# Kernel tuning notes

Measured on AMD Instinct MI355X. Metric: run time of the kernel, lower is better.

Reference implementation:

```python
import jax, jax.numpy as jnp
import numpy as np

N = 50000
E = 1600000
IN_CH = 128
HID = 16
HEADS = 8
OUT_CH = 1
NEG_SLOPE = 0.2


def setup_inputs() -> dict:
    key = jax.random.key(0)
    ks = jax.random.split(key, 12)
    x = jax.random.normal(ks[0], (N, IN_CH), dtype=jnp.float32)
    edge_index = jax.random.randint(ks[1], (2, E), 0, N, dtype=jnp.int64)
    s1 = 1.0 / np.sqrt(IN_CH)
    s2 = 1.0 / np.sqrt(HEADS * HID)
    W1 = jax.random.normal(ks[2], (IN_CH, HEADS * HID), dtype=jnp.float32) * s1
    att_src1 = jax.random.normal(ks[3], (HEADS, HID), dtype=jnp.float32) * s1
    att_dst1 = jax.random.normal(ks[4], (HEADS, HID), dtype=jnp.float32) * s1
    b1 = jnp.zeros((HEADS * HID,), dtype=jnp.float32)
    W2 = jax.random.normal(ks[5], (HEADS * HID, OUT_CH), dtype=jnp.float32) * s2
    att_src2 = jax.random.normal(ks[6], (1, OUT_CH), dtype=jnp.float32) * s2
    att_dst2 = jax.random.normal(ks[7], (1, OUT_CH), dtype=jnp.float32) * s2
    b2 = jnp.zeros((OUT_CH,), dtype=jnp.float32)
    return {"x": x, "edge_index": edge_index,
            "W1": W1, "att_src1": att_src1, "att_dst1": att_dst1, "b1": b1,
            "W2": W2, "att_src2": att_src2, "att_dst2": att_dst2, "b2": b2}


def gat_conv(x, src, dst, W, att_src, att_dst, b, heads, concat):
    n = x.shape[0]
    h = (x @ W).reshape(n, heads, -1)               # [N, H, C]
    a_s = jnp.einsum('nhc,hc->nh', h, att_src)      # [N, H]
    a_d = jnp.einsum('nhc,hc->nh', h, att_dst)
    e = jax.nn.leaky_relu(a_s[src] + a_d[dst], NEG_SLOPE)  # [E, H]
    # segment softmax over incoming edges of each dst node
    emax = jax.ops.segment_max(e, dst, num_segments=n)
    p = jnp.exp(e - emax[dst])
    denom = jax.ops.segment_sum(p, dst, num_segments=n)
    alpha = p / (denom[dst] + 1e-16)                 # [E, H]
    msg = h[src] * alpha[:, :, None]                 # [E, H, C]
    out = jax.ops.segment_sum(msg, dst, num_segments=n)  # [N, H, C]
    if concat:
        out = out.reshape(n, -1)
    else:
        out = out.mean(axis=1)
    return out + b


def reference(x, edge_index, W1, att_src1, att_dst1, b1, W2, att_src2, att_dst2, b2):
    n = x.shape[0]
    loops = jnp.arange(n, dtype=edge_index.dtype)
    src = jnp.concatenate([edge_index[0], loops])    # PyG add_self_loops=True
    dst = jnp.concatenate([edge_index[1], loops])
    h = gat_conv(x, src, dst, W1, att_src1, att_dst1, b1, HEADS, True)
    h = jax.nn.elu(h)
    out = gat_conv(h, src, dst, W2, att_src2, att_dst2, b2, 1, False)
    return out
```

## Files before the change

kernel.cpp:

```cpp
#include <hip/hip_runtime.h>
#include <hip/hip_fp16.h>
#include <math.h>

#define N_NODES 50000
#define N_EDGES 1600000
#define NEG 0.2f

#define PB 256
#define CHUNK (N_EDGES / PB)
#define EPT 25
#define BSHIFT 4
#define NBUCK (N_NODES >> BSHIFT)
#define STRIDE 768
#define GEMMB ((N_NODES + 31) / 32)


__global__ __launch_bounds__(256) void scatter_gemm(const int* __restrict__ ei, int* __restrict__ bcnt,
                                                    int* __restrict__ temp,
                                                    const float* __restrict__ x, const float* __restrict__ W1,
                                                    const float* __restrict__ att_s, const float* __restrict__ att_d,
                                                    __half2* __restrict__ h1, float* __restrict__ as1,
                                                    float* __restrict__ ad1) {
    __shared__ union {
        float xs[128][36];
        int cur[NBUCK];
    } u;
    int t = threadIdx.x;
    if (blockIdx.x < PB) {
        int p = blockIdx.x;
        for (int i = t; i < NBUCK; i += 256) u.cur[i] = 0;
        __syncthreads();
        int e0 = p * CHUNK;
        int vc[EPT];
#pragma unroll
        for (int k = 0; k < EPT; ++k) {
            vc[k] = -1;
            int off = t + k * 256;
            if (off < CHUNK) {
                int e = e0 + off;
                int s = ei[e];
                int d = ei[N_EDGES + e];
                vc[k] = s | (d << 16);
                atomicAdd(&u.cur[d >> BSHIFT], 1);
            }
        }
        __syncthreads();
        for (int i = t; i < NBUCK; i += 256) {
            int h = u.cur[i];
            int c = i * STRIDE;
            if (h) c += atomicAdd(&bcnt[i], h);
            u.cur[i] = c;
        }
        __syncthreads();
#pragma unroll
        for (int k = 0; k < EPT; ++k) {
            int v = vc[k];
            if (v != -1) {
                unsigned d = (unsigned)v >> 16;
                int b = d >> BSHIFT;
                int pos = atomicAdd(&u.cur[b], 1);
                if (pos < (b + 1) * STRIDE)
                    temp[pos] = (v & 0xFFFF) | ((d & 15) << 16);
            }
        }
        return;
    }
    int n0 = (blockIdx.x - PB) * 32;
#pragma unroll
    for (int i = 0; i < 16; ++i) {
        int f = i * 256 + t;
        int r = f >> 7, c = f & 127;
        int gr = n0 + r;
        float v = (gr < N_NODES) ? x[(size_t)gr * 128 + c] : 0.f;
        u.xs[c][r] = v;
    }
    __syncthreads();
    int c0 = (t & 31) * 4;
    int r0 = (t >> 5) * 4;
    float acc[4][4];
#pragma unroll
    for (int i = 0; i < 4; ++i)
#pragma unroll
        for (int j = 0; j < 4; ++j) acc[i][j] = 0.f;
#pragma unroll 4
    for (int k = 0; k < 128; ++k) {
        float4 w = *(const float4*)(W1 + k * 128 + c0);
        float4 xr = *(const float4*)(&u.xs[k][r0]);
        float xv[4] = {xr.x, xr.y, xr.z, xr.w};
        float wv[4] = {w.x, w.y, w.z, w.w};
#pragma unroll
        for (int i = 0; i < 4; ++i)
#pragma unroll
            for (int j = 0; j < 4; ++j) acc[i][j] += xv[i] * wv[j];
    }
#pragma unroll
    for (int i = 0; i < 4; ++i) {
        int row = n0 + r0 + i;
        if (row < N_NODES) {
            __half2 p0 = __float22half2_rn(make_float2(acc[i][0], acc[i][1]));
            __half2 p1 = __float22half2_rn(make_float2(acc[i][2], acc[i][3]));
            h1[(size_t)row * 64 + (c0 >> 1)] = p0;
            h1[(size_t)row * 64 + (c0 >> 1) + 1] = p1;
        }
    }
    int head = (t & 31) >> 2;
    float ps[4], pd[4];
#pragma unroll
    for (int i = 0; i < 4; ++i) {
        float s = 0.f, d = 0.f;
#pragma unroll
        for (int j = 0; j < 4; ++j) {
            s += acc[i][j] * att_s[c0 + j];
            d += acc[i][j] * att_d[c0 + j];
        }
        ps[i] = s; pd[i] = d;
    }
#pragma unroll
    for (int i = 0; i < 4; ++i) {
        ps[i] += __shfl_xor(ps[i], 1, 64);
        ps[i] += __shfl_xor(ps[i], 2, 64);
        pd[i] += __shfl_xor(pd[i], 1, 64);
        pd[i] += __shfl_xor(pd[i], 2, 64);
    }
    if ((t & 3) == 0) {
#pragma unroll
        for (int i = 0; i < 4; ++i) {
            int row = n0 + r0 + i;
            if (row < N_NODES) {
                as1[row * 8 + head] = ps[i];
                ad1[row * 8 + head] = pd[i];
            }
        }
    }
}


__device__ __forceinline__ float lrelu(float v) { return fmaxf(v, NEG * v); }

__global__ __launch_bounds__(128) void agg1_kernel(const char* __restrict__ h1c, const char* __restrict__ as1c,
                                                   const float* __restrict__ ad1, const int* __restrict__ temp,
                                                   const int* __restrict__ bcnt, const float* __restrict__ b1,
                                                   const float* __restrict__ W2, float* __restrict__ h2out) {
    __shared__ int lsrc[STRIDE];
    __shared__ int cnt[16];
    __shared__ int cur[16];
    __shared__ int lrp[16];
    int b = blockIdx.x, t = threadIdx.x;
    int base = b * STRIDE;
    int nE = min(bcnt[b], STRIDE);
    if (t < 16) cnt[t] = 0;
    __syncthreads();
    for (int i = t; i < nE; i += 128)
        atomicAdd(&cnt[(unsigned)temp[base + i] >> 16], 1);
    __syncthreads();
    if (t < 16) {
        int v = cnt[t];
        int incl = v;
#pragma unroll
        for (int off = 1; off < 16; off <<= 1) {
            int u = __shfl_up(incl, off, 16);
            if (t >= off) incl += u;
        }
        int excl = incl - v;
        lrp[t] = excl;
        cur[t] = excl;
    }
    __syncthreads();
    for (int i = t; i < nE; i += 128) {
        int v = temp[base + i];
        int pos = atomicAdd(&cur[(unsigned)v >> 16], 1);
        lsrc[pos] = v & 0xFFFF;
    }
    __syncthreads();

    int lane = t & 63;
    int wave = t >> 6;
    int hB = lane >> 3;
    int hP = lane & 7;
    unsigned lane4 = (unsigned)lane << 2;
    unsigned hP4 = (unsigned)hP << 2;
    int bperm_base = hB << 2;
    int prod = lane >> 3;

    for (int kk = 0; kk < 8; ++kk) {
        int k = wave * 8 + kk;
        int n = b * 16 + k;

        float adP = ad1[n * 8 + hP];
        float adC = ad1[n * 8 + hB];
        float asC = *(const float*)(as1c + ((unsigned)n * 32u + ((unsigned)hB << 2)));
        float p_self = __expf(lrelu(asC + adC));
        __half2 hvs = *(const __half2*)(h1c + (((unsigned)n << 8) + lane4));
        float acc0 = p_self * __half2float(__low2half(hvs));
        float acc1 = p_self * __half2float(__high2half(hvs));
        float l = p_self;

        int jb = lrp[k];
        int deg = cnt[k];
        int j = 0;
        for (; j + 8 <= deg; j += 8) {
            int sP = lsrc[jb + j + prod];
            float aP = *(const float*)(as1c + (((unsigned)sP << 5) + hP4));
            float pP = __expf(lrelu(aP + adP));
            int pPi = __float_as_int(pP);
#pragma unroll
            for (int e = 0; e < 8; ++e) {
                int addr = bperm_base + e * 32;
                float p = __int_as_float(__builtin_amdgcn_ds_bpermute(addr, pPi));
                int s = __builtin_amdgcn_ds_bpermute(addr, sP);
                __half2 hv = *(const __half2*)(h1c + (((unsigned)s << 8) + lane4));
                acc0 += p * __half2float(__low2half(hv));
                acc1 += p * __half2float(__high2half(hv));
                l += p;
            }
        }
        if (j < deg) {
            int r = deg - j;
            int sP = 0;
            float pP = 0.f;
            if (j + prod < deg) {
                sP = lsrc[jb + j + prod];
                float aP = *(const float*)(as1c + (((unsigned)sP << 5) + hP4));
                pP = __expf(lrelu(aP + adP));
            }
            int pPi = __float_as_int(pP);
            for (int e = 0; e < r; ++e) {
                int addr = bperm_base + e * 32;
                float p = __int_as_float(__builtin_amdgcn_ds_bpermute(addr, pPi));
                int s = __builtin_amdgcn_ds_bpermute(addr, sP);
                __half2 hv = *(const __half2*)(h1c + (((unsigned)s << 8) + lane4));
                acc0 += p * __half2float(__low2half(hv));
                acc1 += p * __half2float(__high2half(hv));
                l += p;
            }
        }

        float inv = 1.f / (l + 1e-16f);
        int c0 = lane * 2;
        float y0 = acc0 * inv + b1[c0];
        float y1 = acc1 * inv + b1[c0 + 1];
        y0 = y0 > 0.f ? y0 : expm1f(y0);
        y1 = y1 > 0.f ? y1 : expm1f(y1);
        float part = y0 * W2[c0] + y1 * W2[c0 + 1];
#pragma unroll
        for (int off = 32; off; off >>= 1) part += __shfl_down(part, off, 64);
        if (lane == 0) h2out[n] = part;
    }
}


__global__ __launch_bounds__(128) void agg2_kernel(const float* __restrict__ h2, const int* __restrict__ temp,
                                                   const int* __restrict__ bcnt, const float* __restrict__ att_s2,
                                                   const float* __restrict__ att_d2, const float* __restrict__ b2,
                                                   float* __restrict__ out) {
    __shared__ int lsrc[STRIDE];
    __shared__ int cnt[16];
    __shared__ int cur[16];
    __shared__ int lrp[16];
    int b = blockIdx.x, t = threadIdx.x;
    int base = b * STRIDE;
    int nE = min(bcnt[b], STRIDE);
    if (t < 16) cnt[t] = 0;
    __syncthreads();
    for (int i = t; i < nE; i += 128)
        atomicAdd(&cnt[(unsigned)temp[base + i] >> 16], 1);
    __syncthreads();
    if (t < 16) {
        int v = cnt[t];
        int incl = v;
#pragma unroll
        for (int off = 1; off < 16; off <<= 1) {
            int u = __shfl_up(incl, off, 16);
            if (t >= off) incl += u;
        }
        int excl = incl - v;
        lrp[t] = excl;
        cur[t] = excl;
    }
    __syncthreads();
    for (int i = t; i < nE; i += 128) {
        int v = temp[base + i];
        int pos = atomicAdd(&cur[(unsigned)v >> 16], 1);
        lsrc[pos] = v & 0xFFFF;
    }
    __syncthreads();

    float asw = att_s2[0], adw = att_d2[0];
    int lane = t & 63;
    int wave = t >> 6;
    int sub = lane & 7;
    int k = wave * 8 + (lane >> 3);
    int n = b * 16 + k;
    float h2n = h2[n];
    float ad = h2n * adw;
    float acc = 0.f, l = 0.f;
    if (sub == 0) {
        float p = __expf(lrelu(h2n * asw + ad));
        acc = p * h2n;
        l = p;
    }
    int jb = lrp[k];
    int deg = cnt[k];
    for (int jj = sub; jj < deg; jj += 8) {
        int s = lsrc[jb + jj];
        float hs = h2[s];
        float p = __expf(lrelu(hs * asw + ad));
        acc += p * hs;
        l += p;
    }
#pragma unroll
    for (int off = 4; off; off >>= 1) {
        acc += __shfl_down(acc, off, 8);
        l += __shfl_down(l, off, 8);
    }
    if (sub == 0) out[n] = acc / (l + 1e-16f) + b2[0];
}


extern "C" void kernel_launch(void* const* d_in, const int* in_sizes, int n_in,
                              void* d_out, int out_size, void* d_ws, size_t ws_size,
                              hipStream_t stream) {
    const float* x = (const float*)d_in[0];
    const int* ei = (const int*)d_in[1];
    const float* W1 = (const float*)d_in[2];
    const float* att_s1 = (const float*)d_in[3];
    const float* att_d1 = (const float*)d_in[4];
    const float* b1 = (const float*)d_in[5];
    const float* W2 = (const float*)d_in[6];
    const float* att_s2 = (const float*)d_in[7];
    const float* att_d2 = (const float*)d_in[8];
    const float* b2 = (const float*)d_in[9];
    float* out = (float*)d_out;

    char* p = (char*)d_ws;
    auto alloc = [&](size_t bytes) {
        char* q = p;
        p += (bytes + 255) & ~(size_t)255;
        return q;
    };
    int* bcnt = (int*)alloc((size_t)NBUCK * 4);
    int* temp = (int*)alloc((size_t)NBUCK * STRIDE * 4);
    __half2* h1 = (__half2*)alloc((size_t)N_NODES * 128 * 2);
    float* as1 = (float*)alloc((size_t)N_NODES * 8 * 4);
    float* ad1 = (float*)alloc((size_t)N_NODES * 8 * 4);
    float* h2 = (float*)alloc((size_t)N_NODES * 4);

    hipMemsetAsync(bcnt, 0, (size_t)NBUCK * 4, stream);
    scatter_gemm<<<PB + GEMMB, 256, 0, stream>>>(ei, bcnt, temp,
                                                 x, W1, att_s1, att_d1, h1, as1, ad1);
    agg1_kernel<<<NBUCK, 128, 0, stream>>>((const char*)h1, (const char*)as1, ad1, temp, bcnt, b1, W2, h2);
    agg2_kernel<<<NBUCK, 128, 0, stream>>>(h2, temp, bcnt, att_s2, att_d2, b2, out);
}
```

Before: 214.6 us.

## Software-pipeline edge gathers in agg1 and double the block size to 256

In the layer-1 aggregation kernel, the next batch of eight neighbour feature rows and attention scores is prefetched into registers while the current batch is accumulated. Source indices now come straight from LDS rather than via ds_bpermute. The block grows from 128 to 256 threads, so each wave handles 4 destination nodes instead of 8. The aim is to hide gather latency and raise memory-level parallelism, at the cost of more registers per thread, which may reduce occupancy.

```diff
diff --git a/kernel.cpp b/kernel.cpp
--- a/kernel.cpp
+++ b/kernel.cpp
@@ -137,7 +137,7 @@
 
 __device__ __forceinline__ float lrelu(float v) { return fmaxf(v, NEG * v); }
 
-__global__ __launch_bounds__(128) void agg1_kernel(const char* __restrict__ h1c, const char* __restrict__ as1c,
+__global__ __launch_bounds__(256) void agg1_kernel(const char* __restrict__ h1c, const float* __restrict__ as1,
                                                    const float* __restrict__ ad1, const int* __restrict__ temp,
                                                    const int* __restrict__ bcnt, const float* __restrict__ b1,
                                                    const float* __restrict__ W2, float* __restrict__ h2out) {
@@ -150,7 +150,7 @@
     int nE = min(bcnt[b], STRIDE);
     if (t < 16) cnt[t] = 0;
     __syncthreads();
-    for (int i = t; i < nE; i += 128)
+    for (int i = t; i < nE; i += 256)
         atomicAdd(&cnt[(unsigned)temp[base + i] >> 16], 1);
     __syncthreads();
     if (t < 16) {
@@ -166,7 +166,7 @@
         cur[t] = excl;
     }
     __syncthreads();
-    for (int i = t; i < nE; i += 128) {
+    for (int i = t; i < nE; i += 256) {
         int v = temp[base + i];
         int pos = atomicAdd(&cur[(unsigned)v >> 16], 1);
         lsrc[pos] = v & 0xFFFF;
@@ -177,18 +177,17 @@
     int wave = t >> 6;
     int hB = lane >> 3;
     int hP = lane & 7;
+    int prod = lane >> 3;
     unsigned lane4 = (unsigned)lane << 2;
-    unsigned hP4 = (unsigned)hP << 2;
     int bperm_base = hB << 2;
-    int prod = lane >> 3;
-
-    for (int kk = 0; kk < 8; ++kk) {
-        int k = wave * 8 + kk;
+
+    for (int kk = 0; kk < 4; ++kk) {
+        int k = wave * 4 + kk;
         int n = b * 16 + k;
 
         float adP = ad1[n * 8 + hP];
         float adC = ad1[n * 8 + hB];
-        float asC = *(const float*)(as1c + ((unsigned)n * 32u + ((unsigned)hB << 2)));
+        float asC = as1[n * 8 + hB];
         float p_self = __expf(lrelu(asC + adC));
         __half2 hvs = *(const __half2*)(h1c + (((unsigned)n << 8) + lane4));
         float acc0 = p_self * __half2float(__low2half(hvs));
@@ -197,38 +196,58 @@
 
         int jb = lrp[k];
         int deg = cnt[k];
-        int j = 0;
-        for (; j + 8 <= deg; j += 8) {
-            int sP = lsrc[jb + j + prod];
-            float aP = *(const float*)(as1c + (((unsigned)sP << 5) + hP4));
+        int nfull = deg & ~7;
+
+        __half2 hA[8];
+        float aP = 0.f;
+        if (nfull > 0) {
+            int sP = lsrc[jb + prod];
+            aP = as1[(sP << 3) + hP];
+#pragma unroll
+            for (int e = 0; e < 8; ++e) {
+                int s = lsrc[jb + e];
+                hA[e] = *(const __half2*)(h1c + (((unsigned)s << 8) + lane4));
+            }
+        }
+        for (int j = 0; j < nfull; j += 8) {
+            __half2 hN[8];
+            float aN = 0.f;
+            if (j + 8 < nfull) {
+                int sPn = lsrc[jb + j + 8 + prod];
+                aN = as1[(sPn << 3) + hP];
+#pragma unroll
+                for (int e = 0; e < 8; ++e) {
+                    int s = lsrc[jb + j + 8 + e];
+                    hN[e] = *(const __half2*)(h1c + (((unsigned)s << 8) + lane4));
+                }
+            }
             float pP = __expf(lrelu(aP + adP));
             int pPi = __float_as_int(pP);
 #pragma unroll
             for (int e = 0; e < 8; ++e) {
-                int addr = bperm_base + e * 32;
-                float p = __int_as_float(__builtin_amdgcn_ds_bpermute(addr, pPi));
-                int s = __builtin_amdgcn_ds_bpermute(addr, sP);
-                __half2 hv = *(const __half2*)(h1c + (((unsigned)s << 8) + lane4));
-                acc0 += p * __half2float(__low2half(hv));
-                acc1 += p * __half2float(__high2half(hv));
+                float p = __int_as_float(__builtin_amdgcn_ds_bpermute(bperm_base + e * 32, pPi));
+                acc0 += p * __half2float(__low2half(hA[e]));
+                acc1 += p * __half2float(__high2half(hA[e]));
                 l += p;
             }
-        }
+            aP = aN;
+#pragma unroll
+            for (int e = 0; e < 8; ++e) hA[e] = hN[e];
+        }
+        int j = nfull;
         if (j < deg) {
             int r = deg - j;
-            int sP = 0;
             float pP = 0.f;
             if (j + prod < deg) {
-                sP = lsrc[jb + j + prod];
-                float aP = *(const float*)(as1c + (((unsigned)sP << 5) + hP4));
-                pP = __expf(lrelu(aP + adP));
+                int sP = lsrc[jb + j + prod];
+                float a = as1[(sP << 3) + hP];
+                pP = __expf(lrelu(a + adP));
             }
             int pPi = __float_as_int(pP);
             for (int e = 0; e < r; ++e) {
-                int addr = bperm_base + e * 32;
-                float p = __int_as_float(__builtin_amdgcn_ds_bpermute(addr, pPi));
-                int s = __builtin_amdgcn_ds_bpermute(addr, sP);
+                int s = lsrc[jb + j + e];
                 __half2 hv = *(const __half2*)(h1c + (((unsigned)s << 8) + lane4));
+                float p = __int_as_float(__builtin_amdgcn_ds_bpermute(bperm_base + e * 32, pPi));
                 acc0 += p * __half2float(__low2half(hv));
                 acc1 += p * __half2float(__high2half(hv));
                 l += p;
@@ -348,6 +367,6 @@
     hipMemsetAsync(bcnt, 0, (size_t)NBUCK * 4, stream);
     scatter_gemm<<<PB + GEMMB, 256, 0, stream>>>(ei, bcnt, temp,
                                                  x, W1, att_s1, att_d1, h1, as1, ad1);
-    agg1_kernel<<<NBUCK, 128, 0, stream>>>((const char*)h1, (const char*)as1, ad1, temp, bcnt, b1, W2, h2);
+    agg1_kernel<<<NBUCK, 256, 0, stream>>>((const char*)h1, as1, ad1, temp, bcnt, b1, W2, h2);
     agg2_kernel<<<NBUCK, 128, 0, stream>>>(h2, temp, bcnt, att_s2, att_d2, b2, out);
 }
```

Measured after the change: 226.0 us. +5.3%, slower.

## Split h1 into four channel planes and aggregate per plane with sorted adjacency kernel

Applied to the files above, without the earlier changes.

The GEMM now writes h1 and the attention logits into four planes of 32 channels (two heads) each. A new sort kernel does the per-bucket counting sort once and stores ushort adjacency, degrees and offsets, which both aggregation kernels reuse instead of re-sorting. agg1 launches four times as many blocks, one per plane, so each plane's working set is smaller and more likely to stay in cache. Each wave processes four edges at a time across 16-lane groups and adds its partial layer-2 projection into h2 with atomics, which needs an extra memset and an extra kernel launch.

```diff
diff --git a/kernel.cpp b/kernel.cpp
--- a/kernel.cpp
+++ b/kernel.cpp
@@ -14,13 +14,16 @@
 #define STRIDE 768
 #define GEMMB ((N_NODES + 31) / 32)
 
+#define H1PLANE 800000
+#define ASPLANE 100000
+
 
 __global__ __launch_bounds__(256) void scatter_gemm(const int* __restrict__ ei, int* __restrict__ bcnt,
                                                     int* __restrict__ temp,
                                                     const float* __restrict__ x, const float* __restrict__ W1,
                                                     const float* __restrict__ att_s, const float* __restrict__ att_d,
-                                                    __half2* __restrict__ h1, float* __restrict__ as1,
-                                                    float* __restrict__ ad1) {
+                                                    __half2* __restrict__ h1p, float* __restrict__ asp,
+                                                    float* __restrict__ adp) {
     __shared__ union {
         float xs[128][36];
         int cur[NBUCK];
@@ -93,14 +96,17 @@
 #pragma unroll
             for (int j = 0; j < 4; ++j) acc[i][j] += xv[i] * wv[j];
     }
+    int gplane = c0 >> 5;
+    int within = (c0 & 31) >> 1;
 #pragma unroll
     for (int i = 0; i < 4; ++i) {
         int row = n0 + r0 + i;
         if (row < N_NODES) {
             __half2 p0 = __float22half2_rn(make_float2(acc[i][0], acc[i][1]));
             __half2 p1 = __float22half2_rn(make_float2(acc[i][2], acc[i][3]));
-            h1[(size_t)row * 64 + (c0 >> 1)] = p0;
-            h1[(size_t)row * 64 + (c0 >> 1) + 1] = p1;
+            size_t hb = (size_t)gplane * H1PLANE + (size_t)row * 16 + within;
+            h1p[hb] = p0;
+            h1p[hb + 1] = p1;
         }
     }
     int head = (t & 31) >> 2;
@@ -123,24 +129,22 @@
         pd[i] += __shfl_xor(pd[i], 2, 64);
     }
     if ((t & 3) == 0) {
+        int plane = head >> 1, sub = head & 1;
 #pragma unroll
         for (int i = 0; i < 4; ++i) {
             int row = n0 + r0 + i;
             if (row < N_NODES) {
-                as1[row * 8 + head] = ps[i];
-                ad1[row * 8 + head] = pd[i];
+                asp[(size_t)plane * ASPLANE + row * 2 + sub] = ps[i];
+                adp[(size_t)plane * ASPLANE + row * 2 + sub] = pd[i];
             }
         }
     }
 }
 
 
-__device__ __forceinline__ float lrelu(float v) { return fmaxf(v, NEG * v); }
-
-__global__ __launch_bounds__(128) void agg1_kernel(const char* __restrict__ h1c, const char* __restrict__ as1c,
-                                                   const float* __restrict__ ad1, const int* __restrict__ temp,
-                                                   const int* __restrict__ bcnt, const float* __restrict__ b1,
-                                                   const float* __restrict__ W2, float* __restrict__ h2out) {
+__global__ __launch_bounds__(128) void sort_kernel(const int* __restrict__ temp, const int* __restrict__ bcnt,
+                                                   ushort* __restrict__ sadj, int* __restrict__ ndeg,
+                                                   int* __restrict__ noff) {
     __shared__ int lsrc[STRIDE];
     __shared__ int cnt[16];
     __shared__ int cur[16];
@@ -172,125 +176,106 @@
         lsrc[pos] = v & 0xFFFF;
     }
     __syncthreads();
-
+    for (int i = t; i < nE; i += 128)
+        sadj[base + i] = (ushort)lsrc[i];
+    if (t < 16) {
+        ndeg[b * 16 + t] = cnt[t];
+        noff[b * 16 + t] = base + lrp[t];
+    }
+}
+
+
+__device__ __forceinline__ float lrelu(float v) { return fmaxf(v, NEG * v); }
+
+__global__ __launch_bounds__(256) void agg1_kernel(const __half2* __restrict__ h1p, const float* __restrict__ asp,
+                                                   const float* __restrict__ adp, const ushort* __restrict__ sadj,
+                                                   const int* __restrict__ ndeg, const int* __restrict__ noff,
+                                                   const float* __restrict__ b1, const float* __restrict__ W2,
+                                                   float* __restrict__ h2out) {
+    int g = blockIdx.x & 3;
+    int nb = (blockIdx.x >> 2) * 16;
+    int t = threadIdx.x;
     int lane = t & 63;
     int wave = t >> 6;
-    int hB = lane >> 3;
-    int hP = lane & 7;
-    unsigned lane4 = (unsigned)lane << 2;
-    unsigned hP4 = (unsigned)hP << 2;
-    int bperm_base = hB << 2;
-    int prod = lane >> 3;
-
-    for (int kk = 0; kk < 8; ++kk) {
-        int k = wave * 8 + kk;
-        int n = b * 16 + k;
-
-        float adP = ad1[n * 8 + hP];
-        float adC = ad1[n * 8 + hB];
-        float asC = *(const float*)(as1c + ((unsigned)n * 32u + ((unsigned)hB << 2)));
-        float p_self = __expf(lrelu(asC + adC));
-        __half2 hvs = *(const __half2*)(h1c + (((unsigned)n << 8) + lane4));
-        float acc0 = p_self * __half2float(__low2half(hvs));
-        float acc1 = p_self * __half2float(__high2half(hvs));
-        float l = p_self;
-
-        int jb = lrp[k];
-        int deg = cnt[k];
+    int hs = (lane >> 3) & 1;
+    int cl = lane & 15;
+    int e = lane >> 4;
+    bool e0 = (e == 0);
+    const float* aspg = asp + (size_t)g * ASPLANE;
+    const float* adpg = adp + (size_t)g * ASPLANE;
+    const __half2* h1g = h1p + (size_t)g * H1PLANE;
+
+    for (int kk = 0; kk < 4; ++kk) {
+        int n = nb + wave * 4 + kk;
+
+        float adP = adpg[n * 2 + hs];
+        float asC = aspg[n * 2 + hs];
+        float ps = __expf(lrelu(asC + adP));
+        __half2 hvs = h1g[n * 16 + cl];
+        float acc0 = e0 ? ps * __half2float(__low2half(hvs)) : 0.f;
+        float acc1 = e0 ? ps * __half2float(__high2half(hvs)) : 0.f;
+        float l = e0 ? ps : 0.f;
+
+        int jb = noff[n];
+        int deg = ndeg[n];
         int j = 0;
         for (; j + 8 <= deg; j += 8) {
-            int sP = lsrc[jb + j + prod];
-            float aP = *(const float*)(as1c + (((unsigned)sP << 5) + hP4));
-            float pP = __expf(lrelu(aP + adP));
-            int pPi = __float_as_int(pP);
-#pragma unroll
-            for (int e = 0; e < 8; ++e) {
-                int addr = bperm_base + e * 32;
-                float p = __int_as_float(__builtin_amdgcn_ds_bpermute(addr, pPi));
-                int s = __builtin_amdgcn_ds_bpermute(addr, sP);
-                __half2 hv = *(const __half2*)(h1c + (((unsigned)s << 8) + lane4));
-                acc0 += p * __half2float(__low2half(hv));
-                acc1 += p * __half2float(__high2half(hv));
-                l += p;
-            }
-        }
-        if (j < deg) {
-            int r = deg - j;
-            int sP = 0;
-            float pP = 0.f;
-            if (j + prod < deg) {
-                sP = lsrc[jb + j + prod];
-                float aP = *(const float*)(as1c + (((unsigned)sP << 5) + hP4));
-                pP = __expf(lrelu(aP + adP));
-            }
-            int pPi = __float_as_int(pP);
-            for (int e = 0; e < r; ++e) {
-                int addr = bperm_base + e * 32;
-                float p = __int_as_float(__builtin_amdgcn_ds_bpermute(addr, pPi));
-                int s = __builtin_amdgcn_ds_bpermute(addr, sP);
-                __half2 hv = *(const __half2*)(h1c + (((unsigned)s << 8) + lane4));
-                acc0 += p * __half2float(__low2half(hv));
-                acc1 += p * __half2float(__high2half(hv));
-                l += p;
-            }
-        }
+            int sA = sadj[jb + j + e];
+            int sB = sadj[jb + j + 4 + e];
+            float aA = aspg[sA * 2 + hs];
+            float aB = aspg[sB * 2 + hs];
+            __half2 hA = h1g[sA * 16 + cl];
+            __half2 hB = h1g[sB * 16 + cl];
+            float pA = __expf(lrelu(aA + adP));
+            float pB = __expf(lrelu(aB + adP));
+            acc0 += pA * __half2float(__low2half(hA));
+            acc1 += pA * __half2float(__high2half(hA));
+            l += pA;
+            acc0 += pB * __half2float(__low2half(hB));
+            acc1 += pB * __half2float(__high2half(hB));
+            l += pB;
+        }
+        for (; j < deg; j += 4) {
+            int idx = j + e;
+            bool act = idx < deg;
+            int s = act ? (int)sadj[jb + idx] : n;
+            float a = aspg[s * 2 + hs];
+            __half2 hv = h1g[s * 16 + cl];
+            float p = act ? __expf(lrelu(a + adP)) : 0.f;
+            acc0 += p * __half2float(__low2half(hv));
+            acc1 += p * __half2float(__high2half(hv));
+            l += p;
+        }
+
+        acc0 += __shfl_xor(acc0, 16, 64);
+        acc0 += __shfl_xor(acc0, 32, 64);
+        acc1 += __shfl_xor(acc1, 16, 64);
+        acc1 += __shfl_xor(acc1, 32, 64);
+        l += __shfl_xor(l, 16, 64);
+        l += __shfl_xor(l, 32, 64);
 
         float inv = 1.f / (l + 1e-16f);
-        int c0 = lane * 2;
-        float y0 = acc0 * inv + b1[c0];
-        float y1 = acc1 * inv + b1[c0 + 1];
+        int c = g * 32 + cl * 2;
+        float y0 = acc0 * inv + b1[c];
+        float y1 = acc1 * inv + b1[c + 1];
         y0 = y0 > 0.f ? y0 : expm1f(y0);
         y1 = y1 > 0.f ? y1 : expm1f(y1);
-        float part = y0 * W2[c0] + y1 * W2[c0 + 1];
+        float part = e0 ? (y0 * W2[c] + y1 * W2[c + 1]) : 0.f;
 #pragma unroll
         for (int off = 32; off; off >>= 1) part += __shfl_down(part, off, 64);
-        if (lane == 0) h2out[n] = part;
-    }
-}
-
-
-__global__ __launch_bounds__(128) void agg2_kernel(const float* __restrict__ h2, const int* __restrict__ temp,
-                                                   const int* __restrict__ bcnt, const float* __restrict__ att_s2,
-                                                   const float* __restrict__ att_d2, const float* __restrict__ b2,
-                                                   float* __restrict__ out) {
-    __shared__ int lsrc[STRIDE];
-    __shared__ int cnt[16];
-    __shared__ int cur[16];
-    __shared__ int lrp[16];
+        if (lane == 0) atomicAdd(&h2out[n], part);
+    }
+}
+
+
+__global__ __launch_bounds__(128) void agg2_kernel(const float* __restrict__ h2, const ushort* __restrict__ sadj,
+                                                   const int* __restrict__ ndeg, const int* __restrict__ noff,
+                                                   const float* __restrict__ att_s2, const float* __restrict__ att_d2,
+                                                   const float* __restrict__ b2, float* __restrict__ out) {
     int b = blockIdx.x, t = threadIdx.x;
-    int base = b * STRIDE;
-    int nE = min(bcnt[b], STRIDE);
-    if (t < 16) cnt[t] = 0;
-    __syncthreads();
-    for (int i = t; i < nE; i += 128)
-        atomicAdd(&cnt[(unsigned)temp[base + i] >> 16], 1);
-    __syncthreads();
-    if (t < 16) {
-        int v = cnt[t];
-        int incl = v;
-#pragma unroll
-        for (int off = 1; off < 16; off <<= 1) {
-            int u = __shfl_up(incl, off, 16);
-            if (t >= off) incl += u;
-        }
-        int excl = incl - v;
-        lrp[t] = excl;
-        cur[t] = excl;
-    }
-    __syncthreads();
-    for (int i = t; i < nE; i += 128) {
-        int v = temp[base + i];
-        int pos = atomicAdd(&cur[(unsigned)v >> 16], 1);
-        lsrc[pos] = v & 0xFFFF;
-    }
-    __syncthreads();
-
     float asw = att_s2[0], adw = att_d2[0];
-    int lane = t & 63;
-    int wave = t >> 6;
-    int sub = lane & 7;
-    int k = wave * 8 + (lane >> 3);
-    int n = b * 16 + k;
+    int sub = t & 7;
+    int n = b * 16 + (t >> 3);
     float h2n = h2[n];
     float ad = h2n * adw;
     float acc = 0.f, l = 0.f;
@@ -299,13 +284,13 @@
         acc = p * h2n;
         l = p;
     }
-    int jb = lrp[k];
-    int deg = cnt[k];
+    int jb = noff[n];
+    int deg = ndeg[n];
     for (int jj = sub; jj < deg; jj += 8) {
-        int s = lsrc[jb + jj];
-        float hs = h2[s];
-        float p = __expf(lrelu(hs * asw + ad));
-        acc += p * hs;
+        int s = sadj[jb + jj];
+        float hsv = h2[s];
+        float p = __expf(lrelu(hsv * asw + ad));
+        acc += p * hsv;
         l += p;
     }
 #pragma unroll
@@ -340,14 +325,19 @@
     };
     int* bcnt = (int*)alloc((size_t)NBUCK * 4);
     int* temp = (int*)alloc((size_t)NBUCK * STRIDE * 4);
-    __half2* h1 = (__half2*)alloc((size_t)N_NODES * 128 * 2);
-    float* as1 = (float*)alloc((size_t)N_NODES * 8 * 4);
-    float* ad1 = (float*)alloc((size_t)N_NODES * 8 * 4);
+    ushort* sadj = (ushort*)alloc((size_t)NBUCK * STRIDE * 2);
+    int* ndeg = (int*)alloc((size_t)N_NODES * 4);
+    int* noff = (int*)alloc((size_t)N_NODES * 4);
+    __half2* h1p = (__half2*)alloc((size_t)4 * H1PLANE * 4);
+    float* asp = (float*)alloc((size_t)4 * ASPLANE * 4);
+    float* adp = (float*)alloc((size_t)4 * ASPLANE * 4);
     float* h2 = (float*)alloc((size_t)N_NODES * 4);
 
     hipMemsetAsync(bcnt, 0, (size_t)NBUCK * 4, stream);
+    hipMemsetAsync(h2, 0, (size_t)N_NODES * 4, stream);
     scatter_gemm<<<PB + GEMMB, 256, 0, stream>>>(ei, bcnt, temp,
-                                                 x, W1, att_s1, att_d1, h1, as1, ad1);
-    agg1_kernel<<<NBUCK, 128, 0, stream>>>((const char*)h1, (const char*)as1, ad1, temp, bcnt, b1, W2, h2);
-    agg2_kernel<<<NBUCK, 128, 0, stream>>>(h2, temp, bcnt, att_s2, att_d2, b2, out);
-}
+                                                 x, W1, att_s1, att_d1, h1p, asp, adp);
+    sort_kernel<<<NBUCK, 128, 0, stream>>>(temp, bcnt, sadj, ndeg, noff);
+    agg1_kernel<<<NBUCK * 4, 256, 0, stream>>>(h1p, asp, adp, sadj, ndeg, noff, b1, W2, h2);
+    agg2_kernel<<<NBUCK, 128, 0, stream>>>(h2, sadj, ndeg, noff, att_s2, att_d2, b2, out);
+}
```

New measurement: 278.2 us. 1.3x slower.

## Precompute edge attention weights into LDS with padded segments in agg1

Applied to the files above, without the earlier changes.

Layer-1 aggregation is restructured into two phases. First, all threads compute the per-edge, per-head softmax numerators once, using exp2 with attention logits pre-scaled by log2(e). They store these as half-precision values in LDS and accumulate the denominators with LDS atomics. Self loops become explicit entries, and each node's segment is padded to a multiple of 8 that points at a dummy node (zero features, very negative logit). The gather loop then reads 8 sources and weights per step with no bpermute shuffles or tail loop, and the block size doubles to 256. This trades extra LDS use and fp16 rounding of the weights for less redundant exp work and more loads in flight.

```diff
diff --git a/kernel.cpp b/kernel.cpp
--- a/kernel.cpp
+++ b/kernel.cpp
@@ -5,6 +5,7 @@
 #define N_NODES 50000
 #define N_EDGES 1600000
 #define NEG 0.2f
+#define LOG2E 1.44269504f
 
 #define PB 256
 #define CHUNK (N_EDGES / PB)
@@ -65,6 +66,10 @@
         }
         return;
     }
+    if (blockIdx.x == PB) {
+        if (t < 8) as1[N_NODES * 8 + t] = -3.0e38f;
+        if (t < 64) h1[(size_t)N_NODES * 64 + t] = __float22half2_rn(make_float2(0.f, 0.f));
+    }
     int n0 = (blockIdx.x - PB) * 32;
 #pragma unroll
     for (int i = 0; i < 16; ++i) {
@@ -127,8 +132,8 @@
         for (int i = 0; i < 4; ++i) {
             int row = n0 + r0 + i;
             if (row < N_NODES) {
-                as1[row * 8 + head] = ps[i];
-                ad1[row * 8 + head] = pd[i];
+                as1[row * 8 + head] = ps[i] * LOG2E;
+                ad1[row * 8 + head] = pd[i] * LOG2E;
             }
         }
     }
@@ -137,105 +142,130 @@
 
 __device__ __forceinline__ float lrelu(float v) { return fmaxf(v, NEG * v); }
 
-__global__ __launch_bounds__(128) void agg1_kernel(const char* __restrict__ h1c, const char* __restrict__ as1c,
+__global__ __launch_bounds__(256) void agg1_kernel(const __half2* __restrict__ h1, const float* __restrict__ as1,
                                                    const float* __restrict__ ad1, const int* __restrict__ temp,
                                                    const int* __restrict__ bcnt, const float* __restrict__ b1,
                                                    const float* __restrict__ W2, float* __restrict__ h2out) {
     __shared__ int lsrc[STRIDE];
-    __shared__ int cnt[16];
-    __shared__ int cur[16];
-    __shared__ int lrp[16];
+    __shared__ alignas(16) ushort sLDS[STRIDE];
+    __shared__ float4 pLDS4[STRIDE];
+    __shared__ float lsh[128];
+    __shared__ int cnt[16], cur[16], jb16[16], dp16[16];
+    __shared__ int padTot;
+
     int b = blockIdx.x, t = threadIdx.x;
     int base = b * STRIDE;
     int nE = min(bcnt[b], STRIDE);
     if (t < 16) cnt[t] = 0;
-    __syncthreads();
-    for (int i = t; i < nE; i += 128)
+    if (t < 128) lsh[t] = 0.f;
+    __syncthreads();
+    for (int i = t; i < nE; i += 256)
         atomicAdd(&cnt[(unsigned)temp[base + i] >> 16], 1);
     __syncthreads();
     if (t < 16) {
-        int v = cnt[t];
-        int incl = v;
+        int dr = cnt[t] + 1;
+        int p8 = (dr + 7) & ~7;
+        int incl = p8;
 #pragma unroll
         for (int off = 1; off < 16; off <<= 1) {
-            int u = __shfl_up(incl, off, 16);
-            if (t >= off) incl += u;
-        }
-        int excl = incl - v;
-        lrp[t] = excl;
-        cur[t] = excl;
-    }
-    __syncthreads();
-    for (int i = t; i < nE; i += 128) {
+            int uu = __shfl_up(incl, off, 16);
+            if (t >= off) incl += uu;
+        }
+        int excl = incl - p8;
+        int jb = min(excl, STRIDE);
+        int dp = (min(excl + p8, STRIDE) - jb) & ~7;
+        jb16[t] = jb;
+        dp16[t] = dp;
+        cur[t] = excl + 1;
+        int n = b * 16 + t;
+        if (excl < STRIDE) lsrc[excl] = (t << 16) | n;
+        for (int z = excl + dr; z < excl + p8 && z < STRIDE; ++z)
+            lsrc[z] = (t << 16) | N_NODES;
+        if (t == 15) padTot = min(excl + p8, STRIDE);
+    }
+    __syncthreads();
+    for (int i = t; i < nE; i += 256) {
         int v = temp[base + i];
         int pos = atomicAdd(&cur[(unsigned)v >> 16], 1);
-        lsrc[pos] = v & 0xFFFF;
-    }
+        if (pos < STRIDE) lsrc[pos] = v;
+    }
+    __syncthreads();
+
+    int pT = padTot;
+    __half* pH = (__half*)pLDS4;
+    for (int i = t; i < pT; i += 256) {
+        int v = lsrc[i];
+        int s = v & 0xFFFF;
+        int k16 = v >> 16;
+        sLDS[i] = (ushort)s;
+        float4 a0 = *(const float4*)(as1 + s * 8);
+        float4 a1 = *(const float4*)(as1 + s * 8 + 4);
+        const float* adr = ad1 + (size_t)(b * 16 + k16) * 8;
+        float4 d0 = *(const float4*)adr;
+        float4 d1 = *(const float4*)(adr + 4);
+        float pv[8];
+        pv[0] = exp2f(lrelu(a0.x + d0.x));
+        pv[1] = exp2f(lrelu(a0.y + d0.y));
+        pv[2] = exp2f(lrelu(a0.z + d0.z));
+        pv[3] = exp2f(lrelu(a0.w + d0.w));
+        pv[4] = exp2f(lrelu(a1.x + d1.x));
+        pv[5] = exp2f(lrelu(a1.y + d1.y));
+        pv[6] = exp2f(lrelu(a1.z + d1.z));
+        pv[7] = exp2f(lrelu(a1.w + d1.w));
+        __half* pp = pH + ((i >> 3) * 64 + (i & 7));
+#pragma unroll
+        for (int h = 0; h < 8; ++h) {
+            __half ph = __float2half(pv[h]);
+            pp[h * 8] = ph;
+            atomicAdd(&lsh[k16 * 8 + h], __half2float(ph));
+        }
+    }
+    __syncthreads();
+    if (t < 128) lsh[t] = 1.f / (lsh[t] + 1e-16f);
     __syncthreads();
 
     int lane = t & 63;
     int wave = t >> 6;
     int hB = lane >> 3;
-    int hP = lane & 7;
-    unsigned lane4 = (unsigned)lane << 2;
-    unsigned hP4 = (unsigned)hP << 2;
-    int bperm_base = hB << 2;
-    int prod = lane >> 3;
-
-    for (int kk = 0; kk < 8; ++kk) {
-        int k = wave * 8 + kk;
+    for (int kk = 0; kk < 4; ++kk) {
+        int k = wave * 4 + kk;
         int n = b * 16 + k;
-
-        float adP = ad1[n * 8 + hP];
-        float adC = ad1[n * 8 + hB];
-        float asC = *(const float*)(as1c + ((unsigned)n * 32u + ((unsigned)hB << 2)));
-        float p_self = __expf(lrelu(asC + adC));
-        __half2 hvs = *(const __half2*)(h1c + (((unsigned)n << 8) + lane4));
-        float acc0 = p_self * __half2float(__low2half(hvs));
-        float acc1 = p_self * __half2float(__high2half(hvs));
-        float l = p_self;
-
-        int jb = lrp[k];
-        int deg = cnt[k];
-        int j = 0;
-        for (; j + 8 <= deg; j += 8) {
-            int sP = lsrc[jb + j + prod];
-            float aP = *(const float*)(as1c + (((unsigned)sP << 5) + hP4));
-            float pP = __expf(lrelu(aP + adP));
-            int pPi = __float_as_int(pP);
-#pragma unroll
-            for (int e = 0; e < 8; ++e) {
-                int addr = bperm_base + e * 32;
-                float p = __int_as_float(__builtin_amdgcn_ds_bpermute(addr, pPi));
-                int s = __builtin_amdgcn_ds_bpermute(addr, sP);
-                __half2 hv = *(const __half2*)(h1c + (((unsigned)s << 8) + lane4));
-                acc0 += p * __half2float(__low2half(hv));
-                acc1 += p * __half2float(__high2half(hv));
-                l += p;
-            }
-        }
-        if (j < deg) {
-            int r = deg - j;
-            int sP = 0;
-            float pP = 0.f;
-            if (j + prod < deg) {
-                sP = lsrc[jb + j + prod];
-                float aP = *(const float*)(as1c + (((unsigned)sP << 5) + hP4));
-                pP = __expf(lrelu(aP + adP));
-            }
-            int pPi = __float_as_int(pP);
-            for (int e = 0; e < r; ++e) {
-                int addr = bperm_base + e * 32;
-                float p = __int_as_float(__builtin_amdgcn_ds_bpermute(addr, pPi));
-                int s = __builtin_amdgcn_ds_bpermute(addr, sP);
-                __half2 hv = *(const __half2*)(h1c + (((unsigned)s << 8) + lane4));
-                acc0 += p * __half2float(__low2half(hv));
-                acc1 += p * __half2float(__high2half(hv));
-                l += p;
-            }
-        }
-
-        float inv = 1.f / (l + 1e-16f);
+        int jb = jb16[k], dp = dp16[k];
+        float acc0 = 0.f, acc1 = 0.f;
+        for (int j = 0; j < dp; j += 8) {
+            int4 sv = *(const int4*)&sLDS[jb + j];
+            float4 pf = pLDS4[((jb + j) >> 3) * 8 + hB];
+            const __half* ph = (const __half*)&pf;
+            int s0 = sv.x & 0xFFFF, s1 = (unsigned)sv.x >> 16;
+            int s2 = sv.y & 0xFFFF, s3 = (unsigned)sv.y >> 16;
+            int s4 = sv.z & 0xFFFF, s5 = (unsigned)sv.z >> 16;
+            int s6 = sv.w & 0xFFFF, s7 = (unsigned)sv.w >> 16;
+            __half2 h0 = h1[(unsigned)s0 * 64 + lane];
+            __half2 h1v = h1[(unsigned)s1 * 64 + lane];
+            __half2 h2v = h1[(unsigned)s2 * 64 + lane];
+            __half2 h3 = h1[(unsigned)s3 * 64 + lane];
+            __half2 h4 = h1[(unsigned)s4 * 64 + lane];
+            __half2 h5 = h1[(unsigned)s5 * 64 + lane];
+            __half2 h6 = h1[(unsigned)s6 * 64 + lane];
+            __half2 h7 = h1[(unsigned)s7 * 64 + lane];
+            acc0 += __half2float(ph[0]) * __half2float(__low2half(h0));
+            acc1 += __half2float(ph[0]) * __half2float(__high2half(h0));
+            acc0 += __half2float(ph[1]) * __half2float(__low2half(h1v));
+            acc1 += __half2float(ph[1]) * __half2float(__high2half(h1v));
+            acc0 += __half2float(ph[2]) * __half2float(__low2half(h2v));
+            acc1 += __half2float(ph[2]) * __half2float(__high2half(h2v));
+            acc0 += __half2float(ph[3]) * __half2float(__low2half(h3));
+            acc1 += __half2float(ph[3]) * __half2float(__high2half(h3));
+            acc0 += __half2float(ph[4]) * __half2float(__low2half(h4));
+            acc1 += __half2float(ph[4]) * __half2float(__high2half(h4));
+            acc0 += __half2float(ph[5]) * __half2float(__low2half(h5));
+            acc1 += __half2float(ph[5]) * __half2float(__high2half(h5));
+            acc0 += __half2float(ph[6]) * __half2float(__low2half(h6));
+            acc1 += __half2float(ph[6]) * __half2float(__high2half(h6));
+            acc0 += __half2float(ph[7]) * __half2float(__low2half(h7));
+            acc1 += __half2float(ph[7]) * __half2float(__high2half(h7));
+        }
+        float inv = lsh[k * 8 + hB];
         int c0 = lane * 2;
         float y0 = acc0 * inv + b1[c0];
         float y1 = acc1 * inv + b1[c0 + 1];
@@ -340,14 +370,14 @@
     };
     int* bcnt = (int*)alloc((size_t)NBUCK * 4);
     int* temp = (int*)alloc((size_t)NBUCK * STRIDE * 4);
-    __half2* h1 = (__half2*)alloc((size_t)N_NODES * 128 * 2);
-    float* as1 = (float*)alloc((size_t)N_NODES * 8 * 4);
+    __half2* h1 = (__half2*)alloc((size_t)(N_NODES + 1) * 128 * 2);
+    float* as1 = (float*)alloc(((size_t)N_NODES * 8 + 8) * 4);
     float* ad1 = (float*)alloc((size_t)N_NODES * 8 * 4);
     float* h2 = (float*)alloc((size_t)N_NODES * 4);
 
     hipMemsetAsync(bcnt, 0, (size_t)NBUCK * 4, stream);
     scatter_gemm<<<PB + GEMMB, 256, 0, stream>>>(ei, bcnt, temp,
                                                  x, W1, att_s1, att_d1, h1, as1, ad1);
-    agg1_kernel<<<NBUCK, 128, 0, stream>>>((const char*)h1, (const char*)as1, ad1, temp, bcnt, b1, W2, h2);
+    agg1_kernel<<<NBUCK, 256, 0, stream>>>(h1, as1, ad1, temp, bcnt, b1, W2, h2);
     agg2_kernel<<<NBUCK, 128, 0, stream>>>(h2, temp, bcnt, att_s2, att_d2, b2, out);
 }
```

Measured after the change: 284.3 us. 1.32x slower.
